# Optimization experiments

Hardware: AMD Instinct MI355X
Metric: run time of the kernel (lower is better)

## Reference

```python
import jax, jax.numpy as jnp
import numpy as np

B, S, E, H = 2, 2048, 1024, 16
DK = E // H  # 64


def setup_inputs() -> dict:
    key = jax.random.key(0)
    ks = jax.random.split(key, 5)
    scale = 1.0 / np.sqrt(E)
    return {
        "x": jax.random.normal(ks[0], (B, S, E), dtype=jnp.float32),
        "Wq": jax.random.normal(ks[1], (E, E), dtype=jnp.float32) * scale,
        "Wk": jax.random.normal(ks[2], (E, E), dtype=jnp.float32) * scale,
        "Wv": jax.random.normal(ks[3], (E, E), dtype=jnp.float32) * scale,
        "Wo": jax.random.normal(ks[4], (E, E), dtype=jnp.float32) * scale,
    }


def reference(x, Wq, Wk, Wv, Wo):
    # Linear layers: y = x @ W.T (torch nn.Linear convention, bias=False)
    b, s, e = x.shape
    q = (x @ Wq.T).reshape(b, s, H, DK)  # (B,S,H,dk)
    k = (x @ Wk.T).reshape(b, s, H, DK)
    v = (x @ Wv.T).reshape(b, s, H, DK)
    # scores = Q K^T / sqrt(d_k)  -> (B,H,Sq,Sk)
    scores = jnp.einsum("bihd,bkhd->bhik", q, k) / jnp.sqrt(jnp.asarray(DK, x.dtype))
    p = jax.nn.softmax(scores, axis=-1)
    # dropout is identity in eval/deterministic mode
    attn = jnp.einsum("bhik,bkhd->bihd", p, v)  # (B,S,H,dk)
    concat = attn.reshape(b, s, e)
    return concat @ Wo.T
```

## Files before the change

kernel.cpp:

```cpp
#include <hip/hip_runtime.h>
#include <hip/hip_bf16.h>
#include <cstdint>
#include <cstddef>

typedef __bf16 bf16_t;
typedef __attribute__((ext_vector_type(8))) __bf16 bf16x8;
typedef __attribute__((ext_vector_type(4))) __bf16 bf16x4;
typedef __attribute__((ext_vector_type(4))) float f32x4;
typedef __attribute__((ext_vector_type(16))) float f32x16;
typedef uint32_t u32;
typedef __attribute__((ext_vector_type(4))) u32 u32x4;
typedef __attribute__((ext_vector_type(2))) u32 u32x2;

constexpr int B_ = 2, S_ = 2048, E_ = 1024, H_ = 16, DK_ = 64;

__device__ __forceinline__ void gl2lds16(const void* g, void* l) {
  __builtin_amdgcn_global_load_lds(
      (const __attribute__((address_space(1))) void*)g,
      (__attribute__((address_space(3))) void*)l, 16, 0, 0);
}

__device__ __forceinline__ float exp2_(float x) {
#if __has_builtin(__builtin_amdgcn_exp2f)
  return __builtin_amdgcn_exp2f(x);
#else
  return exp2f(x);
#endif
}

__device__ __forceinline__ u32 cvtpk(float lo, float hi) {
  u32 r;
  asm("v_cvt_pk_bf16_f32 %0, %1, %2" : "=v"(r) : "v"(lo), "v"(hi));
  return r;
}

__device__ __forceinline__ void pl32swap(u32& a, u32& b) {
#if __has_builtin(__builtin_amdgcn_permlane32_swap)
  const u32x2 r = __builtin_amdgcn_permlane32_swap(a, b, false, false);
  a = r[0]; b = r[1];
#else
  asm volatile("v_permlane32_swap_b32 %0, %1" : "+v"(a), "+v"(b));
#endif
}

__device__ __forceinline__ bf16x8 ldsfrag(const char* base, int row, int chunk) {
  return *reinterpret_cast<const bf16x8*>(base + row * 128 + (((chunk ^ (row & 7))) << 4));
}

__global__ __launch_bounds__(256) void f2bf_all(const float* __restrict__ x,
                                                const float* __restrict__ w0,
                                                const float* __restrict__ w1,
                                                const float* __restrict__ w2,
                                                const float* __restrict__ w3,
                                                bf16_t* __restrict__ out) {
  const int i = blockIdx.x * 256 + threadIdx.x;
  const float* src;
  int off;
  if (i < (1 << 20)) {
    src = x; off = i;
  } else {
    const int j = i - (1 << 20);
    const int s = j >> 18;
    off = j & 262143;
    src = s == 0 ? w0 : s == 1 ? w1 : s == 2 ? w2 : w3;
  }
  const float4 v = reinterpret_cast<const float4*>(src)[off];
  bf16x4 o;
  o[0] = (bf16_t)v.x; o[1] = (bf16_t)v.y; o[2] = (bf16_t)v.z; o[3] = (bf16_t)v.w;
  reinterpret_cast<bf16x4*>(out)[i] = o;
}

__global__ __launch_bounds__(256) void gemm_qkv(const bf16_t* __restrict__ A,
                                                const bf16_t* __restrict__ Bt,
                                                bf16_t* __restrict__ Qo,
                                                bf16_t* __restrict__ Ko,
                                                bf16_t* __restrict__ Vto,
                                                float qscale) {
  __shared__ bf16_t As[2][128 * 32];
  __shared__ bf16_t Bs[2][128 * 32];
  const int tid = threadIdx.x;
  const int w = tid >> 6, l = tid & 63;
  const int wr = w >> 1, wc = w & 1;
  const int tm = blockIdx.x * 128, tn = blockIdx.y * 128;
  constexpr int K = 1024, nk = K / 32;
  f32x4 acc[4][4] = {};

  auto stage = [&](int k0, int buf) {
#pragma unroll
    for (int i = 0; i < 2; ++i) {
      const int r = i * 64 + w * 16 + (l >> 2);
      const int c = k0 + (l & 3) * 8;
      gl2lds16(A + (size_t)(tm + r) * K + c, As[buf] + (i * 64 + w * 16) * 32);
      gl2lds16(Bt + (size_t)(tn + r) * K + c, Bs[buf] + (i * 64 + w * 16) * 32);
    }
  };

  stage(0, 0);
  stage(32, 1);

  for (int t = 0; t < nk; ++t) {
    const int cur = t & 1;
    if (t + 1 < nk) asm volatile("s_waitcnt vmcnt(4)" ::: "memory");
    else            asm volatile("s_waitcnt vmcnt(0)" ::: "memory");
    __builtin_amdgcn_s_barrier();
    __builtin_amdgcn_sched_barrier(0);

    bf16x8 af[4], bfr[4];
#pragma unroll
    for (int mi = 0; mi < 4; ++mi)
      af[mi] = *reinterpret_cast<const bf16x8*>(
          As[cur] + (wr * 64 + mi * 16 + (l & 15)) * 32 + (l >> 4) * 8);
#pragma unroll
    for (int ni = 0; ni < 4; ++ni)
      bfr[ni] = *reinterpret_cast<const bf16x8*>(
          Bs[cur] + (wc * 64 + ni * 16 + (l & 15)) * 32 + (l >> 4) * 8);
#pragma unroll
    for (int mi = 0; mi < 4; ++mi)
#pragma unroll
      for (int ni = 0; ni < 4; ++ni)
        acc[mi][ni] =
            __builtin_amdgcn_mfma_f32_16x16x32_bf16(af[mi], bfr[ni], acc[mi][ni], 0, 0, 0);

    if (t + 2 < nk) {
      __builtin_amdgcn_s_barrier();
      __builtin_amdgcn_sched_barrier(0);
      stage((t + 2) * 32, cur);
    }
  }

#pragma unroll
  for (int mi = 0; mi < 4; ++mi)
#pragma unroll
    for (int ni = 0; ni < 4; ++ni) {
      if (tn < 2048) {
        bf16_t* C = (tn < 1024) ? Qo : Ko;
        const float sc = (tn < 1024) ? qscale : 1.0f;
        const int colb = (tn < 1024) ? tn : tn - 1024;
#pragma unroll
        for (int r = 0; r < 4; ++r) {
          const int row = tm + wr * 64 + mi * 16 + (l >> 4) * 4 + r;
          const int col = colb + wc * 64 + ni * 16 + (l & 15);
          C[(size_t)row * 1024 + col] = (bf16_t)(acc[mi][ni][r] * sc);
        }
      } else {
        const int tok0 = tm + wr * 64 + mi * 16 + (l >> 4) * 4;
        const int feat = (tn - 2048) + wc * 64 + ni * 16 + (l & 15);
        const int b = tok0 >> 11, s = tok0 & 2047;
        bf16x4 o4;
#pragma unroll
        for (int r = 0; r < 4; ++r) o4[r] = (bf16_t)acc[mi][ni][r];
        *reinterpret_cast<bf16x4*>(Vto + (((size_t)(b * E_ + feat)) << 11) + s) = o4;
      }
    }
}

__global__ __launch_bounds__(256) void gemm_o(const bf16_t* __restrict__ A,
                                              const bf16_t* __restrict__ Bt,
                                              float* __restrict__ C) {
  __shared__ bf16_t As[2][64 * 32];
  __shared__ bf16_t Bs[2][128 * 32];
  const int tid = threadIdx.x;
  const int w = tid >> 6, l = tid & 63;
  const int wr = w >> 1, wc = w & 1;
  const int tm = blockIdx.x * 64, tn = blockIdx.y * 128;
  constexpr int K = 1024, nk = K / 32;
  f32x4 acc[2][4] = {};

  auto stage = [&](int k0, int buf) {
    const int c = k0 + (l & 3) * 8;
    gl2lds16(A + (size_t)(tm + w * 16 + (l >> 2)) * K + c, As[buf] + (w * 16) * 32);
#pragma unroll
    for (int i = 0; i < 2; ++i)
      gl2lds16(Bt + (size_t)(tn + i * 64 + w * 16 + (l >> 2)) * K + c,
               Bs[buf] + (i * 64 + w * 16) * 32);
  };

  stage(0, 0);
  stage(32, 1);

  for (int t = 0; t < nk; ++t) {
    const int cur = t & 1;
    if (t + 1 < nk) asm volatile("s_waitcnt vmcnt(3)" ::: "memory");
    else            asm volatile("s_waitcnt vmcnt(0)" ::: "memory");
    __builtin_amdgcn_s_barrier();
    __builtin_amdgcn_sched_barrier(0);

    bf16x8 af[2], bfr[4];
#pragma unroll
    for (int mi = 0; mi < 2; ++mi)
      af[mi] = *reinterpret_cast<const bf16x8*>(
          As[cur] + (wr * 32 + mi * 16 + (l & 15)) * 32 + (l >> 4) * 8);
#pragma unroll
    for (int ni = 0; ni < 4; ++ni)
      bfr[ni] = *reinterpret_cast<const bf16x8*>(
          Bs[cur] + (wc * 64 + ni * 16 + (l & 15)) * 32 + (l >> 4) * 8);
#pragma unroll
    for (int mi = 0; mi < 2; ++mi)
#pragma unroll
      for (int ni = 0; ni < 4; ++ni)
        acc[mi][ni] =
            __builtin_amdgcn_mfma_f32_16x16x32_bf16(af[mi], bfr[ni], acc[mi][ni], 0, 0, 0);

    if (t + 2 < nk) {
      __builtin_amdgcn_s_barrier();
      __builtin_amdgcn_sched_barrier(0);
      stage((t + 2) * 32, cur);
    }
  }

#pragma unroll
  for (int mi = 0; mi < 2; ++mi)
#pragma unroll
    for (int ni = 0; ni < 4; ++ni)
#pragma unroll
      for (int r = 0; r < 4; ++r) {
        const int row = tm + wr * 32 + mi * 16 + (l >> 4) * 4 + r;
        const int col = tn + wc * 64 + ni * 16 + (l & 15);
        C[(size_t)row * 1024 + col] = acc[mi][ni][r];
      }
}

template <int NSPL>
__global__ __launch_bounds__(256, 2) void attn_fwd(const bf16_t* __restrict__ Q,
                                                   const bf16_t* __restrict__ K,
                                                   const bf16_t* __restrict__ Vt,
                                                   bf16_t* __restrict__ O,
                                                   u32* __restrict__ Op,
                                                   float* __restrict__ lbuf) {
  __shared__ __align__(16) char smem[32768];
  const int tid = threadIdx.x;
  const int w = tid >> 6, l = tid & 63;
  const int hi = l >> 5, l31 = l & 31;
  const int nblk = 512 * NSPL;
  const int flat = blockIdx.x;
  const int wid = (flat & 7) * (nblk >> 3) + (flat >> 3);
  const int qb = wid & 15, bh = (wid >> 4) & 31;
  const int part = wid >> 9;
  const int q0 = qb * 128 + w * 32;
  const size_t hb = (size_t)(bh >> 4) * (S_ * E_) + (size_t)(bh & 15) * DK_;
  const bf16_t* const Qh = Q + hb;
  const bf16_t* const Kh = K + hb;
  const bf16_t* const Vth = Vt + (size_t)bh * (DK_ * S_);

  const int srow = l >> 3;
  const int schunk = (l & 7) ^ srow;

  bf16x8 ones;
  {
    u32x4 ow;
    ow[0] = 0x3F803F80u; ow[1] = 0x3F803F80u; ow[2] = 0x3F803F80u; ow[3] = 0x3F803F80u;
    ones = __builtin_bit_cast(bf16x8, ow);
  }
  f32x16 m12;
#pragma unroll
  for (int u = 0; u < 16; ++u) m12[u] = -12.0f;

  bf16x8 qf[4];
#pragma unroll
  for (int df = 0; df < 4; ++df)
    qf[df] = *reinterpret_cast<const bf16x8*>(
        Qh + (size_t)(q0 + l31) * E_ + df * 16 + hi * 8);

  f32x16 oacc[2] = {};
  f32x16 lacc = {};

  auto stage = [&](int t, int buf) {
    const int t0 = t * 64;
#pragma unroll
    for (int i = 0; i < 2; ++i) {
      const int rg = w * 2 + i;
      const int row = rg * 8 + srow;
      gl2lds16(Kh + (size_t)(t0 + row) * E_ + schunk * 8,
               smem + buf * 8192 + rg * 1024);
      gl2lds16(Vth + (size_t)row * S_ + t0 + schunk * 8,
               smem + 16384 + buf * 8192 + rg * 1024);
    }
  };

  const int ntl = 32 / NSPL;
  const int tbeg = part * ntl;

  stage(tbeg, 0);
  stage(tbeg + 1, 1);

  for (int tt = 0; tt < ntl; ++tt) {
    const int cur = tt & 1;
    if (tt + 1 < ntl) asm volatile("s_waitcnt vmcnt(4)" ::: "memory");
    else              asm volatile("s_waitcnt vmcnt(0)" ::: "memory");
    __builtin_amdgcn_s_barrier();
    __builtin_amdgcn_sched_barrier(0);

    const char* const Kcur = smem + cur * 8192;
    const char* const Vcur = smem + 16384 + cur * 8192;

    f32x16 sacc[2];
    __builtin_amdgcn_s_setprio(1);
#pragma unroll
    for (int kb = 0; kb < 2; ++kb) {
      {
        const bf16x8 kf = ldsfrag(Kcur, kb * 32 + l31, hi);
        sacc[kb] = __builtin_amdgcn_mfma_f32_32x32x16_bf16(kf, qf[0], m12, 0, 0, 0);
      }
#pragma unroll
      for (int df = 1; df < 4; ++df) {
        const bf16x8 kf = ldsfrag(Kcur, kb * 32 + l31, df * 2 + hi);
        sacc[kb] = __builtin_amdgcn_mfma_f32_32x32x16_bf16(kf, qf[df], sacc[kb], 0, 0, 0);
      }
    }
    __builtin_amdgcn_s_setprio(0);

#pragma unroll
    for (int kb = 0; kb < 2; ++kb)
#pragma unroll
      for (int u = 0; u < 16; ++u)
        sacc[kb][u] = exp2_(sacc[kb][u]);

#pragma unroll
    for (int kf = 0; kf < 4; ++kf) {
      const int kb = kf >> 1, u0 = (kf & 1) * 8;
      u32 w0 = cvtpk(sacc[kb][u0 + 0], sacc[kb][u0 + 1]);
      u32 w1 = cvtpk(sacc[kb][u0 + 2], sacc[kb][u0 + 3]);
      u32 w2 = cvtpk(sacc[kb][u0 + 4], sacc[kb][u0 + 5]);
      u32 w3 = cvtpk(sacc[kb][u0 + 6], sacc[kb][u0 + 7]);
      pl32swap(w0, w2);
      pl32swap(w1, w3);
      u32x4 pw; pw[0] = w0; pw[1] = w1; pw[2] = w2; pw[3] = w3;
      const bf16x8 pa = __builtin_bit_cast(bf16x8, pw);
      __builtin_amdgcn_s_setprio(1);
#pragma unroll
      for (int dn = 0; dn < 2; ++dn) {
        const bf16x8 vf = ldsfrag(Vcur, dn * 32 + l31, kf * 2 + hi);
        oacc[dn] = __builtin_amdgcn_mfma_f32_32x32x16_bf16(pa, vf, oacc[dn], 0, 0, 0);
      }
      lacc = __builtin_amdgcn_mfma_f32_32x32x16_bf16(pa, ones, lacc, 0, 0, 0);
      __builtin_amdgcn_s_setprio(0);
    }

    if (tt + 2 < ntl) {
      __builtin_amdgcn_s_barrier();
      __builtin_amdgcn_sched_barrier(0);
      stage(tbeg + tt + 2, cur);
    }
  }

  if constexpr (NSPL > 1) {
    const int pb = part * 65536 + bh * S_;
#pragma unroll
    for (int u = 0; u < 16; ++u) {
      if (l31 == u) {
        const int q = q0 + (u & 3) + 8 * (u >> 2) + 4 * hi;
        lbuf[pb + q] = lacc[u];
      }
    }
    u32* const Oph = Op + (size_t)part * 2097152 + (size_t)(bh * S_) * 32 + l31;
#pragma unroll
    for (int u = 0; u < 16; ++u) {
      const int q = q0 + (u & 3) + 8 * (u >> 2) + 4 * hi;
      Oph[(size_t)q * 32] = cvtpk(oacc[0][u], oacc[1][u]);
    }
  } else {
#pragma unroll
    for (int u = 0; u < 16; ++u) {
      const float inv = 1.f / lacc[u];
      const int q = q0 + (u & 3) + 8 * (u >> 2) + 4 * hi;
      O[hb + (size_t)q * E_ + l31] = (bf16_t)(oacc[0][u] * inv);
      O[hb + (size_t)q * E_ + 32 + l31] = (bf16_t)(oacc[1][u] * inv);
    }
  }
}

__global__ __launch_bounds__(256) void attn_combine(const u32* __restrict__ Op,
                                                    const float* __restrict__ lbuf,
                                                    bf16_t* __restrict__ Ac) {
  const int idx = blockIdx.x * 256 + threadIdx.x;
  const int r = idx >> 5, c = idx & 31;
  const float lsum = lbuf[r] + lbuf[65536 + r];
  float o0 = 0.f, o1 = 0.f;
#pragma unroll
  for (int i = 0; i < 2; ++i) {
    const u32 p = Op[(size_t)i * 2097152 + (size_t)r * 32 + c];
    o0 += __builtin_bit_cast(float, p << 16);
    o1 += __builtin_bit_cast(float, p & 0xFFFF0000u);
  }
  const float inv = 1.f / lsum;
  const int q = r & 2047, bh = r >> 11;
  bf16_t* const base =
      Ac + (size_t)(bh >> 4) * (S_ * E_) + (size_t)q * E_ + (bh & 15) * DK_;
  base[c] = (bf16_t)(o0 * inv);
  base[c + 32] = (bf16_t)(o1 * inv);
}

extern "C" void kernel_launch(void* const* d_in, const int* in_sizes, int n_in,
                              void* d_out, int out_size, void* d_ws, size_t ws_size,
                              hipStream_t stream) {
  const float* x  = (const float*)d_in[0];
  const float* Wq = (const float*)d_in[1];
  const float* Wk = (const float*)d_in[2];
  const float* Wv = (const float*)d_in[3];
  const float* Wo = (const float*)d_in[4];
  float* out = (float*)d_out;

  bf16_t* xb  = (bf16_t*)d_ws;
  bf16_t* wqb = xb + 4194304;
  bf16_t* wob = wqb + 3145728;
  bf16_t* Qb  = wqb + 4194304;
  bf16_t* Kb  = Qb + 4194304;
  bf16_t* Vtb = Kb + 4194304;
  u32*    Opart = (u32*)(Vtb + 4194304);
  float*  lbuf  = (float*)d_ws;

  const bool split = ws_size >= 76546048ull;

  f2bf_all<<<8192, 256, 0, stream>>>(x, Wq, Wk, Wv, Wo, xb);

  gemm_qkv<<<dim3(32, 24), 256, 0, stream>>>(xb, wqb, Qb, Kb, Vtb, 0.18033688f);

  if (split) {
    bf16_t* Ac = Kb;
    attn_fwd<2><<<1024, 256, 0, stream>>>(Qb, Kb, Vtb, nullptr, Opart, lbuf);
    attn_combine<<<8192, 256, 0, stream>>>(Opart, lbuf, Ac);
    gemm_o<<<dim3(64, 8), 256, 0, stream>>>(Ac, wob, out);
  } else {
    bf16_t* Ac = xb;
    attn_fwd<1><<<512, 256, 0, stream>>>(Qb, Kb, Vtb, Ac, nullptr, nullptr);
    gemm_o<<<dim3(64, 8), 256, 0, stream>>>(Ac, wob, out);
  }
}
```

Before: 117.2 us.

## Fuse split-attention combine into output projection GEMM A-tile loading

Removes the separate attn_combine kernel and instead merges the two split-K attention partials, normalizes by the summed softmax denominators, and converts to bf16 while staging the A tile inside a new gemm_o_cmb kernel. This saves one launch and the write and re-read of the combined attention buffer. In exchange the GEMM's A loads go through registers instead of direct global-to-LDS copies. Each A element is re-read and re-combined by all 8 column-tile blocks, and the pipeline uses manual barriers that could stall more.

After: 115.5 us, median of 2. Within noise of the previous version (-1.4%).

```diff
diff --git a/kernel.cpp b/kernel.cpp
--- a/kernel.cpp
+++ b/kernel.cpp
@@ -152,6 +152,134 @@
         *reinterpret_cast<bf16x4*>(Vto + (((size_t)(b * E_ + feat)) << 11) + s) = o4;
       }
     }
+}
+
+__global__ __launch_bounds__(256) void gemm_o_cmb(const u32* __restrict__ Op,
+                                                  const float* __restrict__ lbuf,
+                                                  const bf16_t* __restrict__ Bt,
+                                                  float* __restrict__ C) {
+  __shared__ bf16_t As[2][64 * 32];
+  __shared__ bf16_t Bs[2][128 * 32];
+  const int tid = threadIdx.x;
+  const int w = tid >> 6, l = tid & 63;
+  const int wr = w >> 1, wc = w & 1;
+  const int tm = blockIdx.x * 64, tn = blockIdx.y * 128;
+  f32x4 acc[2][4] = {};
+
+  const int t4 = tid & 3;
+  const int arow = tm + (tid >> 2);
+  const int b = arow >> 11, q = arow & 2047;
+
+  auto loadA = [&](int s, u32x4& a0, u32x4& a1, u32x4& c0, u32x4& c1,
+                   float& l0, float& l1) {
+    const int head = s >> 1;
+    const size_t r = (size_t)((b << 4) + head) * 2048 + q;
+    const u32* p0 = Op + r * 32 + t4 * 8;
+    const u32* p1 = Op + 2097152 + r * 32 + t4 * 8;
+    a0 = *reinterpret_cast<const u32x4*>(p0);
+    a1 = *reinterpret_cast<const u32x4*>(p0 + 4);
+    c0 = *reinterpret_cast<const u32x4*>(p1);
+    c1 = *reinterpret_cast<const u32x4*>(p1 + 4);
+    l0 = lbuf[r];
+    l1 = lbuf[65536 + r];
+  };
+  auto convA = [&](const u32x4& a0, const u32x4& a1, const u32x4& c0, const u32x4& c1,
+                   float l0, float l1, int buf, bool hi16) {
+    const float inv = 1.f / (l0 + l1);
+    float o[8];
+#pragma unroll
+    for (int j = 0; j < 4; ++j) {
+      const u32 u0 = a0[j], v0 = c0[j], u1 = a1[j], v1 = c1[j];
+      o[j] = (hi16 ? (__builtin_bit_cast(float, u0 & 0xFFFF0000u) +
+                      __builtin_bit_cast(float, v0 & 0xFFFF0000u))
+                   : (__builtin_bit_cast(float, u0 << 16) +
+                      __builtin_bit_cast(float, v0 << 16))) * inv;
+      o[j + 4] = (hi16 ? (__builtin_bit_cast(float, u1 & 0xFFFF0000u) +
+                          __builtin_bit_cast(float, v1 & 0xFFFF0000u))
+                       : (__builtin_bit_cast(float, u1 << 16) +
+                          __builtin_bit_cast(float, v1 << 16))) * inv;
+    }
+    u32x4 pk;
+    pk[0] = cvtpk(o[0], o[1]); pk[1] = cvtpk(o[2], o[3]);
+    pk[2] = cvtpk(o[4], o[5]); pk[3] = cvtpk(o[6], o[7]);
+    *reinterpret_cast<u32x4*>(As[buf] + (tid >> 2) * 32 + t4 * 8) = pk;
+  };
+  auto loadB = [&](int s, bf16x8& v0, bf16x8& v1) {
+    const int c = s * 32 + (l & 3) * 8;
+    v0 = *reinterpret_cast<const bf16x8*>(
+        Bt + (size_t)(tn + w * 16 + (l >> 2)) * 1024 + c);
+    v1 = *reinterpret_cast<const bf16x8*>(
+        Bt + (size_t)(tn + 64 + w * 16 + (l >> 2)) * 1024 + c);
+  };
+  auto writeB = [&](int buf, const bf16x8& v0, const bf16x8& v1) {
+    *reinterpret_cast<bf16x8*>(Bs[buf] + (w * 16 + (l >> 2)) * 32 + (l & 3) * 8) = v0;
+    *reinterpret_cast<bf16x8*>(Bs[buf] + (64 + w * 16 + (l >> 2)) * 32 + (l & 3) * 8) = v1;
+  };
+  auto compute = [&](int buf) {
+    bf16x8 af[2], bfr[4];
+#pragma unroll
+    for (int mi = 0; mi < 2; ++mi)
+      af[mi] = *reinterpret_cast<const bf16x8*>(
+          As[buf] + (wr * 32 + mi * 16 + (l & 15)) * 32 + (l >> 4) * 8);
+#pragma unroll
+    for (int ni = 0; ni < 4; ++ni)
+      bfr[ni] = *reinterpret_cast<const bf16x8*>(
+          Bs[buf] + (wc * 64 + ni * 16 + (l & 15)) * 32 + (l >> 4) * 8);
+#pragma unroll
+    for (int mi = 0; mi < 2; ++mi)
+#pragma unroll
+      for (int ni = 0; ni < 4; ++ni)
+        acc[mi][ni] =
+            __builtin_amdgcn_mfma_f32_16x16x32_bf16(af[mi], bfr[ni], acc[mi][ni], 0, 0, 0);
+  };
+
+  {
+    u32x4 ta, tb, tc, td; float tl0, tl1; bf16x8 v0, v1;
+    loadA(0, ta, tb, tc, td, tl0, tl1); loadB(0, v0, v1);
+    convA(ta, tb, tc, td, tl0, tl1, 0, false); writeB(0, v0, v1);
+    loadA(1, ta, tb, tc, td, tl0, tl1); loadB(1, v0, v1);
+    convA(ta, tb, tc, td, tl0, tl1, 1, true); writeB(1, v0, v1);
+  }
+  u32x4 A0a, A0b, A0c, A0d; float A0l0, A0l1; bf16x8 B0a, B0b;
+  u32x4 A1a, A1b, A1c, A1d; float A1l0, A1l1; bf16x8 B1a, B1b;
+  loadA(2, A0a, A0b, A0c, A0d, A0l0, A0l1); loadB(2, B0a, B0b);
+  loadA(3, A1a, A1b, A1c, A1d, A1l0, A1l1); loadB(3, B1a, B1b);
+
+  for (int t = 0; t < 32; t += 2) {
+    asm volatile("s_waitcnt lgkmcnt(0)" ::: "memory");
+    __builtin_amdgcn_s_barrier();
+    __builtin_amdgcn_sched_barrier(0);
+    compute(0);
+    if (t + 2 < 32) {
+      __builtin_amdgcn_s_barrier();
+      __builtin_amdgcn_sched_barrier(0);
+      convA(A0a, A0b, A0c, A0d, A0l0, A0l1, 0, false);
+      writeB(0, B0a, B0b);
+      if (t + 4 < 32) { loadA(t + 4, A0a, A0b, A0c, A0d, A0l0, A0l1); loadB(t + 4, B0a, B0b); }
+    }
+    asm volatile("s_waitcnt lgkmcnt(0)" ::: "memory");
+    __builtin_amdgcn_s_barrier();
+    __builtin_amdgcn_sched_barrier(0);
+    compute(1);
+    if (t + 3 < 32) {
+      __builtin_amdgcn_s_barrier();
+      __builtin_amdgcn_sched_barrier(0);
+      convA(A1a, A1b, A1c, A1d, A1l0, A1l1, 1, true);
+      writeB(1, B1a, B1b);
+      if (t + 5 < 32) { loadA(t + 5, A1a, A1b, A1c, A1d, A1l0, A1l1); loadB(t + 5, B1a, B1b); }
+    }
+  }
+
+#pragma unroll
+  for (int mi = 0; mi < 2; ++mi)
+#pragma unroll
+    for (int ni = 0; ni < 4; ++ni)
+#pragma unroll
+      for (int r = 0; r < 4; ++r) {
+        const int row = tm + wr * 32 + mi * 16 + (l >> 4) * 4 + r;
+        const int col = tn + wc * 64 + ni * 16 + (l & 15);
+        C[(size_t)row * 1024 + col] = acc[mi][ni][r];
+      }
 }
 
 __global__ __launch_bounds__(256) void gemm_o(const bf16_t* __restrict__ A,
@@ -369,27 +497,6 @@
   }
 }
 
-__global__ __launch_bounds__(256) void attn_combine(const u32* __restrict__ Op,
-                                                    const float* __restrict__ lbuf,
-                                                    bf16_t* __restrict__ Ac) {
-  const int idx = blockIdx.x * 256 + threadIdx.x;
-  const int r = idx >> 5, c = idx & 31;
-  const float lsum = lbuf[r] + lbuf[65536 + r];
-  float o0 = 0.f, o1 = 0.f;
-#pragma unroll
-  for (int i = 0; i < 2; ++i) {
-    const u32 p = Op[(size_t)i * 2097152 + (size_t)r * 32 + c];
-    o0 += __builtin_bit_cast(float, p << 16);
-    o1 += __builtin_bit_cast(float, p & 0xFFFF0000u);
-  }
-  const float inv = 1.f / lsum;
-  const int q = r & 2047, bh = r >> 11;
-  bf16_t* const base =
-      Ac + (size_t)(bh >> 4) * (S_ * E_) + (size_t)q * E_ + (bh & 15) * DK_;
-  base[c] = (bf16_t)(o0 * inv);
-  base[c + 32] = (bf16_t)(o1 * inv);
-}
-
 extern "C" void kernel_launch(void* const* d_in, const int* in_sizes, int n_in,
                               void* d_out, int out_size, void* d_ws, size_t ws_size,
                               hipStream_t stream) {
@@ -416,10 +523,8 @@
   gemm_qkv<<<dim3(32, 24), 256, 0, stream>>>(xb, wqb, Qb, Kb, Vtb, 0.18033688f);
 
   if (split) {
-    bf16_t* Ac = Kb;
     attn_fwd<2><<<1024, 256, 0, stream>>>(Qb, Kb, Vtb, nullptr, Opart, lbuf);
-    attn_combine<<<8192, 256, 0, stream>>>(Opart, lbuf, Ac);
-    gemm_o<<<dim3(64, 8), 256, 0, stream>>>(Ac, wob, out);
+    gemm_o_cmb<<<dim3(64, 8), 256, 0, stream>>>(Opart, lbuf, wob, out);
   } else {
     bf16_t* Ac = xb;
     attn_fwd<1><<<512, 256, 0, stream>>>(Qb, Kb, Vtb, Ac, nullptr, nullptr);
```
